# Kernel optimization log

Hardware: AMD Instinct MI355X
Metric: run time of the kernel (lower is better)

The kernel has to match this reference:

```python
import jax, jax.numpy as jnp
import numpy as np

INPUT_SIZE = 128
HIDDEN_SIZE = 1024
OUTPUT_SIZE = 64
E_PROP = 0.8
E_SIZE = int(E_PROP * HIDDEN_SIZE)  # 819
I_SIZE = HIDDEN_SIZE - E_SIZE       # 205


def _make_mask():
    # rows of [+1]*E_SIZE + [-1]*I_SIZE, zero diagonal (no self-connection)
    row = np.concatenate([np.ones(E_SIZE), -np.ones(I_SIZE)]).astype(np.float32)
    mask = np.tile(row, (HIDDEN_SIZE, 1))
    np.fill_diagonal(mask, 0.0)
    return jnp.asarray(mask)


def setup_inputs() -> dict:
    key = jax.random.key(0)
    ks = jax.random.split(key, 8)
    T, B = 512, 64
    scale = 1.0 / np.sqrt(HIDDEN_SIZE)
    x = jax.random.normal(ks[0], (T, B, INPUT_SIZE), dtype=jnp.float32)
    w_ih = jax.random.normal(ks[1], (HIDDEN_SIZE, INPUT_SIZE), dtype=jnp.float32) / np.sqrt(INPUT_SIZE)
    b_ih = jax.random.uniform(ks[2], (HIDDEN_SIZE,), minval=-scale, maxval=scale, dtype=jnp.float32)
    w_hh = jax.random.normal(ks[3], (HIDDEN_SIZE, HIDDEN_SIZE), dtype=jnp.float32) * scale
    # mimic reset_parameters: shrink excitatory columns by e_size/i_size ratio
    w_hh = w_hh.at[:, :E_SIZE].divide(E_SIZE / I_SIZE)
    b_hh = jax.random.uniform(ks[4], (HIDDEN_SIZE,), minval=-scale, maxval=scale, dtype=jnp.float32)
    w_fc = jax.random.normal(ks[5], (OUTPUT_SIZE, E_SIZE), dtype=jnp.float32) / np.sqrt(E_SIZE)
    b_fc = jax.random.uniform(ks[6], (OUTPUT_SIZE,), minval=-scale, maxval=scale, dtype=jnp.float32)
    # NOTE: RNN.__init__ hard-codes alpha = 1 regardless of the value passed in.
    alpha = jnp.array([1.0], dtype=jnp.float32)
    mask = _make_mask()
    return {"x": x, "w_ih": w_ih, "b_ih": b_ih, "w_hh": w_hh, "b_hh": b_hh,
            "w_fc": w_fc, "b_fc": b_fc, "alpha": alpha, "mask": mask}


def reference(x, w_ih, b_ih, w_hh, b_hh, w_fc, b_fc, alpha, mask):
    # x: (T, B, I). Precompute input projection for all timesteps (one big GEMM).
    inp_proj = jnp.einsum('tbi,hi->tbh', x, w_ih) + b_ih  # (T, B, H)
    # effective E-I weight: sign-constrained, zero diagonal; constant across steps
    eff_w = jnp.abs(w_hh) * mask                           # (H, H)
    a = alpha[0]
    B = x.shape[1]
    state0 = jnp.zeros((B, HIDDEN_SIZE), dtype=x.dtype)
    out0 = jnp.zeros((B, HIDDEN_SIZE), dtype=x.dtype)

    def step(carry, u_t):
        state, output = carry
        total = u_t + output @ eff_w.T + b_hh             # (B, H)
        state = a * (total - state) + state               # alpha blend (sigma_rec = 0)
        output = jnp.tanh(state)
        return (state, output), output

    _, rnn_activity = jax.lax.scan(step, (state0, out0), inp_proj)  # (T, B, H)
    rnn_e = rnn_activity[:, :, :E_SIZE]                   # excitatory readout only
    out = jnp.einsum('tbe,oe->tbo', rnn_e, w_fc) + b_fc   # (T, B, O)
    return out, rnn_activity
```

## Files before the change

### kernel.cpp

```cpp
#include <hip/hip_runtime.h>
#include <cmath>

#define T_STEPS 512
#define BATCH   64
#define HID     1024
#define INSZ    128
#define ESZ     819
#define OSZ     64

#define WS_EFFW   0
#define WS_WIHT   1048576
#define WS_HIST   1179648
#define WS_BADJ   34734080
#define WS_WFCP   34742272

typedef float f32x4 __attribute__((ext_vector_type(4)));

__global__ void prep_effw(const float* __restrict__ w_hh, const float* __restrict__ mask,
                          float* __restrict__ eff) {
    const int i = (blockIdx.x * 256 + threadIdx.x) * 4;
    const float4 w = *(const float4*)(w_hh + i);
    const float4 m = *(const float4*)(mask + i);
    float4 r;
    r.x = fabsf(w.x) * m.x; r.y = fabsf(w.y) * m.y;
    r.z = fabsf(w.z) * m.z; r.w = fabsf(w.w) * m.w;
    *(float4*)(eff + i) = r;
}

__global__ void prep_wihT(const float* __restrict__ w_ih, float* __restrict__ w_ihT) {
    const int idx = blockIdx.x * 256 + threadIdx.x;
    const int i = idx >> 10, h = idx & 1023;
    w_ihT[idx] = w_ih[h * INSZ + i];
}

__global__ void prep_wfc(const float* __restrict__ w_fc, const float* __restrict__ b_fc,
                         float* __restrict__ w_fcp, float* __restrict__ badj) {
    __shared__ float red[256];
    const int o = blockIdx.x, tid = threadIdx.x;
    float s = 0.f;
    for (int e = tid; e < 820; e += 256) {
        const float w = (e < ESZ) ? w_fc[o * ESZ + e] : 0.f;
        w_fcp[o * 820 + e] = w;
        s += w;
    }
    red[tid] = s;
    __syncthreads();
    for (int st = 128; st; st >>= 1) {
        if (tid < st) red[tid] += red[tid + st];
        __syncthreads();
    }
    if (tid == 0) badj[o] = b_fc[o] - 2.0f * red[0];
}

__global__ void inp_proj(const float* __restrict__ x, const float* __restrict__ w_ihT,
                         const float* __restrict__ b_ih, float* __restrict__ u) {
    __shared__ float xs[INSZ * 64];
    const int t = blockIdx.x, tid = threadIdx.x;
    const float* xt = x + (size_t)t * BATCH * INSZ;
    for (int k = tid * 4; k < BATCH * INSZ; k += 1024) {
        const float4 v = *(const float4*)(xt + k);
        const int b = k >> 7, i = k & 127;
        xs[(i + 0) * 64 + b] = v.x; xs[(i + 1) * 64 + b] = v.y;
        xs[(i + 2) * 64 + b] = v.z; xs[(i + 3) * 64 + b] = v.w;
    }
    __syncthreads();
    for (int hp = 0; hp < 2; ++hp) {
        const int h = hp * 512 + tid * 2;
        const float bi0 = b_ih[h], bi1 = b_ih[h + 1];
        for (int b0 = 0; b0 < 64; b0 += 8) {
            float acc0[8], acc1[8];
#pragma unroll
            for (int bb = 0; bb < 8; ++bb) { acc0[bb] = 0.f; acc1[bb] = 0.f; }
#pragma unroll 4
            for (int i = 0; i < INSZ; ++i) {
                const float2 w2 = *(const float2*)(w_ihT + i * 1024 + h);
                const float4 xa = *(const float4*)(xs + i * 64 + b0);
                const float4 xb = *(const float4*)(xs + i * 64 + b0 + 4);
                const float xv[8] = {xa.x, xa.y, xa.z, xa.w, xb.x, xb.y, xb.z, xb.w};
#pragma unroll
                for (int bb = 0; bb < 8; ++bb) {
                    acc0[bb] = fmaf(w2.x, xv[bb], acc0[bb]);
                    acc1[bb] = fmaf(w2.y, xv[bb], acc1[bb]);
                }
            }
#pragma unroll
            for (int bb = 0; bb < 8; ++bb) {
                float2 r; r.x = acc0[bb] + bi0; r.y = acc1[bb] + bi1;
                *(float2*)(u + ((size_t)(b0 + bb) * T_STEPS + t) * 1024 + h) = r;
            }
        }
    }
}

#define ISSUE2(VA, VB, SRC)                                               \
    asm volatile("global_load_dwordx4 %0, %2, off sc0\n\t"                \
                 "global_load_dwordx4 %1, %2, off offset:512 sc0"         \
                 : "=&v"(VA), "=&v"(VB) : "v"(SRC) : "memory")
#define WAIT2(VA, VB)                                                     \
    asm volatile("s_waitcnt vmcnt(0)" : "+v"(VA), "+v"(VB) :: "memory")
#define RELOAD2(VA, VB, SRC)                                              \
    asm volatile("global_load_dwordx4 %0, %2, off sc0 sc1\n\t"            \
                 "global_load_dwordx4 %1, %2, off offset:512 sc0 sc1\n\t" \
                 "s_waitcnt vmcnt(0)"                                     \
                 : "=&v"(VA), "=&v"(VB) : "v"(SRC) : "memory")

#define RAWBAR()                                                          \
    do { asm volatile("s_waitcnt lgkmcnt(0)" ::: "memory");               \
         __builtin_amdgcn_s_barrier(); } while (0)

__device__ __forceinline__ float min8f(f32x4 x, f32x4 y) {
    return fminf(fminf(fminf(x[0], x[1]), fminf(x[2], x[3])),
                 fminf(fminf(y[0], y[1]), fminf(y[2], y[3])));
}

__global__ void __launch_bounds__(256, 1)
rnn_scan(const float* __restrict__ eff_w, const float* __restrict__ u,
         const float* __restrict__ b_hh, const float* __restrict__ alpha,
         float* __restrict__ hist) {
    extern __shared__ float smem[];
    float* w_s = smem;
    float* pp  = smem + 32768;
    const int tid = threadIdx.x, wg = blockIdx.x;
    const int bg = wg & 7, hgrp = wg >> 3;
    const int h0 = hgrp << 5, b0 = bg << 3;

    float rsum = 0.f;
    {
        const int hl = tid >> 3, grp = hl >> 2, l4 = hl & 3;
        const int j0 = (tid & 7) << 7;
        const float* wrow = eff_w + (size_t)(h0 + hl) * 1024;
        for (int j = j0; j < j0 + 128; j += 4) {
            const float4 w4 = *(const float4*)(wrow + j);
            w_s[((j + 0) << 5) + (((grp + j + 0) & 7) << 2) + l4] = w4.x;
            w_s[((j + 1) << 5) + (((grp + j + 1) & 7) << 2) + l4] = w4.y;
            w_s[((j + 2) << 5) + (((grp + j + 2) & 7) << 2) + l4] = w4.z;
            w_s[((j + 3) << 5) + (((grp + j + 3) & 7) << 2) + l4] = w4.w;
            rsum += (w4.x + w4.y) + (w4.z + w4.w);
        }
    }
    rsum += __shfl_xor(rsum, 1);
    rsum += __shfl_xor(rsum, 2);
    rsum += __shfl_xor(rsum, 4);

    const float a = alpha[0];
    const int r_hl = tid >> 3, r_b = tid & 7;
    const int rh = h0 + r_hl, rb = b0 + r_b;
    const float bias0 = b_hh[rh];
    const float bias_eff = bias0 - 2.0f * rsum;
    const size_t u_base = ((size_t)rb * T_STEPS) * 1024 + rh;
    float* const my_hist = hist + ((size_t)rb * T_STEPS) * 1024 + rh;
    const int hp = tid >> 5, jc = tid & 31;
    const int b_s = tid >> 5, q = tid & 31;
    const float* const sbase = hist + ((size_t)(b0 + b_s) * T_STEPS) * 1024 + (q << 2);
    const int s1 = ((q & 7) + (q >> 3)) & 7;
    const int s2 = (s1 + 4) & 7;
    const int ppA = (b_s << 10) + ((q >> 3) << 5) + (s1 << 2);
    const int ppB = (b_s << 10) + 128 + ((q >> 3) << 5) + (s2 << 2);
    const int cbase = ((hgrp >> 3) + 1) & 3;
    float state = 0.f;
    f32x4 vA, vB;
    __syncthreads();

    for (int t = 0; t < T_STEPS; ++t) {
        const float uval = u[u_base + ((size_t)t << 10)];
        float red = 0.f;
        if (t > 0) {
            const float* srow = sbase + ((size_t)(t - 1) << 10);
            float A[32];
#pragma unroll
            for (int i = 0; i < 32; ++i) A[i] = 0.f;

            int cc = cbase;
            for (int k = 0; k < 4; ++k) {
                {
                    const float* sc = srow + (cc << 8);
                    WAIT2(vA, vB);
                    float mn = min8f(vA, vB);
                    while (!(mn >= 1.0f)) {
                        __builtin_amdgcn_s_sleep(1);
                        RELOAD2(vA, vB, sc);
                        mn = min8f(vA, vB);
                    }
                    *(f32x4*)(pp + (cc << 8) + ppA) = vA;
                    *(f32x4*)(pp + (cc << 8) + ppB) = vB;
                }
                RAWBAR();
                if (k < 3) { const float* nsrc = srow + ((((cc + 1) & 3)) << 8); ISSUE2(vA, vB, nsrc); }
#pragma unroll
                for (int l = 0; l < 8; ++l) {
                    const int jjg = (cc << 3) + l;
                    const int j = (jjg << 5) + jc;
                    const f32x4 wv = *(const f32x4*)&w_s[(j << 5) + (((hp + j) & 7) << 2)];
                    const int phij = (jjg << 5) + ((((jc >> 2) + jjg) & 7) << 2) + (jc & 3);
                    float pv[8];
#pragma unroll
                    for (int b = 0; b < 8; ++b) pv[b] = pp[(b << 10) + phij];
#pragma unroll
                    for (int b = 0; b < 8; ++b) {
                        A[0 * 8 + b] = fmaf(wv[0], pv[b], A[0 * 8 + b]);
                        A[1 * 8 + b] = fmaf(wv[1], pv[b], A[1 * 8 + b]);
                        A[2 * 8 + b] = fmaf(wv[2], pv[b], A[2 * 8 + b]);
                        A[3 * 8 + b] = fmaf(wv[3], pv[b], A[3 * 8 + b]);
                    }
                }
                cc = (cc + 1) & 3;
            }
#pragma unroll
            for (int r = 0; r < 16; ++r) {
                const float give = (tid & 16) ? A[r] : A[r + 16];
                const float keep = (tid & 16) ? A[r + 16] : A[r];
                A[r] = keep + __shfl_xor(give, 16, 64);
            }
#pragma unroll
            for (int r = 0; r < 8; ++r) {
                const float give = (tid & 8) ? A[r] : A[r + 8];
                const float keep = (tid & 8) ? A[r + 8] : A[r];
                A[r] = keep + __shfl_xor(give, 8, 64);
            }
#pragma unroll
            for (int r = 0; r < 4; ++r) {
                const float give = (tid & 4) ? A[r] : A[r + 4];
                const float keep = (tid & 4) ? A[r + 4] : A[r];
                A[r] = keep + __shfl_xor(give, 4, 64);
            }
#pragma unroll
            for (int r = 0; r < 2; ++r) {
                const float give = (tid & 2) ? A[r] : A[r + 2];
                const float keep = (tid & 2) ? A[r + 2] : A[r];
                A[r] = keep + __shfl_xor(give, 2, 64);
            }
            {
                const float give = (tid & 1) ? A[0] : A[1];
                const float keep = (tid & 1) ? A[1] : A[0];
                A[0] = keep + __shfl_xor(give, 1, 64);
            }
            red = A[0];
        }
        const float tot = uval + red + ((t > 0) ? bias_eff : bias0);
        state = fmaf(a, tot - state, state);
        const float ov = tanhf(state);
        __hip_atomic_store(my_hist + ((size_t)t << 10), ov + 2.0f, __ATOMIC_RELAXED,
                           __HIP_MEMORY_SCOPE_AGENT);
        { const float* nsrc = sbase + ((size_t)t << 10) + (cbase << 8); ISSUE2(vA, vB, nsrc); }
        RAWBAR();
    }
}

__global__ void copy_act(const float* __restrict__ hist, float* __restrict__ act) {
    const int t = blockIdx.x >> 6, b = blockIdx.x & 63;
    const float* src = hist + ((size_t)b * T_STEPS + t) * 1024 + threadIdx.x * 4;
    float* dst = act + ((size_t)t * BATCH + b) * 1024 + threadIdx.x * 4;
    float4 v = *(const float4*)src;
    v.x -= 2.0f; v.y -= 2.0f; v.z -= 2.0f; v.w -= 2.0f;
    *(float4*)dst = v;
}

__global__ void fc_out(const float* __restrict__ hist, const float* __restrict__ w_fcp,
                       const float* __restrict__ badj, float* __restrict__ out0) {
    __shared__ float hs[16 * 820];
    const int t = blockIdx.x >> 2, bq = blockIdx.x & 3, tid = threadIdx.x;
    const int b0 = bq << 4;
    for (int r = 0; r < 16; ++r) {
        const float* src = hist + ((size_t)(b0 + r) * T_STEPS + t) * 1024;
        for (int e = tid; e < 820; e += 256) hs[r * 820 + e] = (e < ESZ) ? src[e] : 0.f;
    }
    __syncthreads();
    const int bb = tid >> 4, ol = tid & 15;
    float acc[4] = {0.f, 0.f, 0.f, 0.f};
    const float* hrow = hs + bb * 820;
    for (int e = 0; e < 820; e += 4) {
        const float4 hv = *(const float4*)(hrow + e);
#pragma unroll
        for (int k = 0; k < 4; ++k) {
            const float4 wv = *(const float4*)(w_fcp + (size_t)(ol + (k << 4)) * 820 + e);
            acc[k] += hv.x * wv.x + hv.y * wv.y + hv.z * wv.z + hv.w * wv.w;
        }
    }
    const int b = b0 + bb;
#pragma unroll
    for (int k = 0; k < 4; ++k) {
        const int o = ol + (k << 4);
        out0[((size_t)t * BATCH + b) * OSZ + o] = acc[k] + badj[o];
    }
}

extern "C" void kernel_launch(void* const* d_in, const int* in_sizes, int n_in,
                              void* d_out, int out_size, void* d_ws, size_t ws_size,
                              hipStream_t stream) {
    const float* x     = (const float*)d_in[0];
    const float* w_ih  = (const float*)d_in[1];
    const float* b_ih  = (const float*)d_in[2];
    const float* w_hh  = (const float*)d_in[3];
    const float* b_hh  = (const float*)d_in[4];
    const float* w_fc  = (const float*)d_in[5];
    const float* b_fc  = (const float*)d_in[6];
    const float* alpha = (const float*)d_in[7];
    const float* mask  = (const float*)d_in[8];

    float* out  = (float*)d_out;
    float* out0 = out;
    float* act  = out + (size_t)T_STEPS * BATCH * OSZ;

    float* ws     = (float*)d_ws;
    float* eff_w  = ws + WS_EFFW;
    float* w_ihT  = ws + WS_WIHT;
    float* hist   = ws + WS_HIST;
    float* badj   = ws + WS_BADJ;
    float* w_fcp  = ws + WS_WFCP;
    float* u      = act;

    hipMemsetAsync(hist, 0, (size_t)BATCH * T_STEPS * HID * sizeof(float), stream);
    prep_effw<<<1024, 256, 0, stream>>>(w_hh, mask, eff_w);
    prep_wihT<<<512, 256, 0, stream>>>(w_ih, w_ihT);
    prep_wfc<<<64, 256, 0, stream>>>(w_fc, b_fc, w_fcp, badj);
    inp_proj<<<512, 256, 0, stream>>>(x, w_ihT, b_ih, u);

    hipFuncSetAttribute(reinterpret_cast<const void*>(rnn_scan),
                        hipFuncAttributeMaxDynamicSharedMemorySize, 163840);
    void* args[] = {(void*)&eff_w, (void*)&u, (void*)&b_hh, (void*)&alpha, (void*)&hist};
    hipLaunchCooperativeKernel(reinterpret_cast<const void*>(rnn_scan),
                               dim3(256), dim3(256), args, 163840, stream);

    copy_act<<<32768, 256, 0, stream>>>(hist, act);
    fc_out<<<2048, 256, 0, stream>>>(hist, w_fcp, badj, out0);
}
```

Measured before the change: 4.062 ms.

## Replace chunked prefetch-and-compute pipeline with single full-row poll then compute

The per-step cross-workgroup wait is restructured. Before, the previous step's hidden state was fetched in four chunks with prefetching, so computing on one chunk overlapped with polling for the next. Now all eight vector loads (the full 1024-wide row slice) are issued at once and polled with sc0 sc1 cache bypass until every value is ready, followed by a single barrier and one 32-iteration FMA loop. This drops three of the four barriers per step and the staggered chunk order, at the cost of losing overlap between arriving data and compute, and it no longer issues an early prefetch after the store.

```diff
diff --git a/kernel.cpp b/kernel.cpp
--- a/kernel.cpp
+++ b/kernel.cpp
@@ -92,26 +92,30 @@
     }
 }
 
-#define ISSUE2(VA, VB, SRC)                                               \
-    asm volatile("global_load_dwordx4 %0, %2, off sc0\n\t"                \
-                 "global_load_dwordx4 %1, %2, off offset:512 sc0"         \
-                 : "=&v"(VA), "=&v"(VB) : "v"(SRC) : "memory")
-#define WAIT2(VA, VB)                                                     \
-    asm volatile("s_waitcnt vmcnt(0)" : "+v"(VA), "+v"(VB) :: "memory")
-#define RELOAD2(VA, VB, SRC)                                              \
-    asm volatile("global_load_dwordx4 %0, %2, off sc0 sc1\n\t"            \
-                 "global_load_dwordx4 %1, %2, off offset:512 sc0 sc1\n\t" \
-                 "s_waitcnt vmcnt(0)"                                     \
-                 : "=&v"(VA), "=&v"(VB) : "v"(SRC) : "memory")
+#define LOAD8()                                                                \
+    asm volatile("global_load_dwordx4 %0, %8, off sc0 sc1\n\t"                 \
+                 "global_load_dwordx4 %1, %8, off offset:512 sc0 sc1\n\t"      \
+                 "global_load_dwordx4 %2, %8, off offset:1024 sc0 sc1\n\t"     \
+                 "global_load_dwordx4 %3, %8, off offset:1536 sc0 sc1\n\t"     \
+                 "global_load_dwordx4 %4, %8, off offset:2048 sc0 sc1\n\t"     \
+                 "global_load_dwordx4 %5, %8, off offset:2560 sc0 sc1\n\t"     \
+                 "global_load_dwordx4 %6, %8, off offset:3072 sc0 sc1\n\t"     \
+                 "global_load_dwordx4 %7, %8, off offset:3584 sc0 sc1\n\t"     \
+                 "s_waitcnt vmcnt(0)"                                          \
+                 : "=&v"(v0), "=&v"(v1), "=&v"(v2), "=&v"(v3),                 \
+                   "=&v"(v4), "=&v"(v5), "=&v"(v6), "=&v"(v7)                  \
+                 : "v"(srow) : "memory")
+
+__device__ __forceinline__ float vmin4f(f32x4 v) {
+    return fminf(fminf(v[0], v[1]), fminf(v[2], v[3]));
+}
+#define MIN32()                                                                  \
+    fminf(fminf(fminf(vmin4f(v0), vmin4f(v1)), fminf(vmin4f(v2), vmin4f(v3))),   \
+          fminf(fminf(vmin4f(v4), vmin4f(v5)), fminf(vmin4f(v6), vmin4f(v7))))
 
 #define RAWBAR()                                                          \
     do { asm volatile("s_waitcnt lgkmcnt(0)" ::: "memory");               \
          __builtin_amdgcn_s_barrier(); } while (0)
-
-__device__ __forceinline__ float min8f(f32x4 x, f32x4 y) {
-    return fminf(fminf(fminf(x[0], x[1]), fminf(x[2], x[3])),
-                 fminf(fminf(y[0], y[1]), fminf(y[2], y[3])));
-}
 
 __global__ void __launch_bounds__(256, 1)
 rnn_scan(const float* __restrict__ eff_w, const float* __restrict__ u,
@@ -156,9 +160,7 @@
     const int s2 = (s1 + 4) & 7;
     const int ppA = (b_s << 10) + ((q >> 3) << 5) + (s1 << 2);
     const int ppB = (b_s << 10) + 128 + ((q >> 3) << 5) + (s2 << 2);
-    const int cbase = ((hgrp >> 3) + 1) & 3;
     float state = 0.f;
-    f32x4 vA, vB;
     __syncthreads();
 
     for (int t = 0; t < T_STEPS; ++t) {
@@ -166,73 +168,64 @@
         float red = 0.f;
         if (t > 0) {
             const float* srow = sbase + ((size_t)(t - 1) << 10);
+            f32x4 v0, v1, v2, v3, v4, v5, v6, v7;
+            LOAD8();
+            float mn = MIN32();
+            while (!(mn >= 1.0f)) {
+                __builtin_amdgcn_s_sleep(1);
+                LOAD8();
+                mn = MIN32();
+            }
+            {
+                float* dA = pp + ppA; float* dB = pp + ppB;
+                *(f32x4*)(dA + 0)   = v0;  *(f32x4*)(dB + 0)   = v1;
+                *(f32x4*)(dA + 256) = v2;  *(f32x4*)(dB + 256) = v3;
+                *(f32x4*)(dA + 512) = v4;  *(f32x4*)(dB + 512) = v5;
+                *(f32x4*)(dA + 768) = v6;  *(f32x4*)(dB + 768) = v7;
+            }
+            RAWBAR();
             float A[32];
 #pragma unroll
             for (int i = 0; i < 32; ++i) A[i] = 0.f;
-
-            int cc = cbase;
-            for (int k = 0; k < 4; ++k) {
-                {
-                    const float* sc = srow + (cc << 8);
-                    WAIT2(vA, vB);
-                    float mn = min8f(vA, vB);
-                    while (!(mn >= 1.0f)) {
-                        __builtin_amdgcn_s_sleep(1);
-                        RELOAD2(vA, vB, sc);
-                        mn = min8f(vA, vB);
-                    }
-                    *(f32x4*)(pp + (cc << 8) + ppA) = vA;
-                    *(f32x4*)(pp + (cc << 8) + ppB) = vB;
+#pragma unroll 4
+            for (int jj = 0; jj < 32; ++jj) {
+                const int j = (jj << 5) + jc;
+                const f32x4 wv = *(const f32x4*)&w_s[(j << 5) + (((hp + j) & 7) << 2)];
+                const int phij = (jj << 5) + ((((jc >> 2) + jj) & 7) << 2) + (jc & 3);
+                float pv[8];
+#pragma unroll
+                for (int b = 0; b < 8; ++b) pv[b] = pp[(b << 10) + phij];
+#pragma unroll
+                for (int b = 0; b < 8; ++b) {
+                    A[0 * 8 + b] = fmaf(wv[0], pv[b], A[0 * 8 + b]);
+                    A[1 * 8 + b] = fmaf(wv[1], pv[b], A[1 * 8 + b]);
+                    A[2 * 8 + b] = fmaf(wv[2], pv[b], A[2 * 8 + b]);
+                    A[3 * 8 + b] = fmaf(wv[3], pv[b], A[3 * 8 + b]);
                 }
-                RAWBAR();
-                if (k < 3) { const float* nsrc = srow + ((((cc + 1) & 3)) << 8); ISSUE2(vA, vB, nsrc); }
-#pragma unroll
-                for (int l = 0; l < 8; ++l) {
-                    const int jjg = (cc << 3) + l;
-                    const int j = (jjg << 5) + jc;
-                    const f32x4 wv = *(const f32x4*)&w_s[(j << 5) + (((hp + j) & 7) << 2)];
-                    const int phij = (jjg << 5) + ((((jc >> 2) + jjg) & 7) << 2) + (jc & 3);
-                    float pv[8];
-#pragma unroll
-                    for (int b = 0; b < 8; ++b) pv[b] = pp[(b << 10) + phij];
-#pragma unroll
-                    for (int b = 0; b < 8; ++b) {
-                        A[0 * 8 + b] = fmaf(wv[0], pv[b], A[0 * 8 + b]);
-                        A[1 * 8 + b] = fmaf(wv[1], pv[b], A[1 * 8 + b]);
-                        A[2 * 8 + b] = fmaf(wv[2], pv[b], A[2 * 8 + b]);
-                        A[3 * 8 + b] = fmaf(wv[3], pv[b], A[3 * 8 + b]);
-                    }
-                }
-                cc = (cc + 1) & 3;
             }
 #pragma unroll
             for (int r = 0; r < 16; ++r) {
-                const float give = (tid & 16) ? A[r] : A[r + 16];
-                const float keep = (tid & 16) ? A[r + 16] : A[r];
-                A[r] = keep + __shfl_xor(give, 16, 64);
+                const float g = (tid & 16) ? A[r] : A[r + 16], kp = (tid & 16) ? A[r + 16] : A[r];
+                A[r] = kp + __shfl_xor(g, 16, 64);
             }
 #pragma unroll
             for (int r = 0; r < 8; ++r) {
-                const float give = (tid & 8) ? A[r] : A[r + 8];
-                const float keep = (tid & 8) ? A[r + 8] : A[r];
-                A[r] = keep + __shfl_xor(give, 8, 64);
+                const float g = (tid & 8) ? A[r] : A[r + 8], kp = (tid & 8) ? A[r + 8] : A[r];
+                A[r] = kp + __shfl_xor(g, 8, 64);
             }
 #pragma unroll
             for (int r = 0; r < 4; ++r) {
-                const float give = (tid & 4) ? A[r] : A[r + 4];
-                const float keep = (tid & 4) ? A[r + 4] : A[r];
-                A[r] = keep + __shfl_xor(give, 4, 64);
+                const float g = (tid & 4) ? A[r] : A[r + 4], kp = (tid & 4) ? A[r + 4] : A[r];
+                A[r] = kp + __shfl_xor(g, 4, 64);
             }
 #pragma unroll
             for (int r = 0; r < 2; ++r) {
-                const float give = (tid & 2) ? A[r] : A[r + 2];
-                const float keep = (tid & 2) ? A[r + 2] : A[r];
-                A[r] = keep + __shfl_xor(give, 2, 64);
+                const float g = (tid & 2) ? A[r] : A[r + 2], kp = (tid & 2) ? A[r + 2] : A[r];
+                A[r] = kp + __shfl_xor(g, 2, 64);
             }
             {
-                const float give = (tid & 1) ? A[0] : A[1];
-                const float keep = (tid & 1) ? A[1] : A[0];
-                A[0] = keep + __shfl_xor(give, 1, 64);
+                const float g = (tid & 1) ? A[0] : A[1], kp = (tid & 1) ? A[1] : A[0];
+                A[0] = kp + __shfl_xor(g, 1, 64);
             }
             red = A[0];
         }
@@ -241,7 +234,6 @@
         const float ov = tanhf(state);
         __hip_atomic_store(my_hist + ((size_t)t << 10), ov + 2.0f, __ATOMIC_RELAXED,
                            __HIP_MEMORY_SCOPE_AGENT);
-        { const float* nsrc = sbase + ((size_t)t << 10) + (cbase << 8); ISSUE2(vA, vB, nsrc); }
         RAWBAR();
     }
 }
```

Result: slower. 4.752 ms (+17.0%).
